# Performance work log

Measured on AMD Instinct MI355X. Metric: run time of the kernel, lower is better.

## Reference

```python
import jax, jax.numpy as jnp
import numpy as np

B, S, D, H, L, DFF, NA = 128, 52, 1024, 16, 8, 4096, 1000
DK = D // H
KTOP = int((1.0 - 0.9) * S)  # per-row top-k kept before threshold = 5
EPS = 1e-5
SCALE = 1.0 / np.sqrt(DK).astype(np.float32)


def setup_inputs() -> dict:
    key = jax.random.key(0)
    ks = jax.random.split(key, 30)
    # token grid: channels 0,1 in [0,50) so only designated positions match special tokens
    x = jax.random.randint(ks[0], (B, S, 3), 0, 50).astype(jnp.int32)
    act = jax.random.randint(ks[1], (B, S), 0, NA).astype(jnp.int32)
    x = x.at[..., 2].set(act)
    x = x.at[:, 0].set(jnp.array([100, 0, 1], jnp.int32))    # SOS
    x = x.at[:, 26].set(jnp.array([100, 0, 2], jnp.int32))   # SEP
    x = x.at[:, 48:].set(jnp.array([100, 0, 0], jnp.int32))  # PAD tail

    def n(k, shape, scale=0.02):
        return (jax.random.normal(k, shape) * scale).astype(jnp.float32)

    return dict(
        x=x,
        action_emb=n(ks[2], (NA, D), 1.0),
        sep_token=n(ks[3], (D,), 1.0),
        bn_gamma=jnp.ones((S,), jnp.float32),
        bn_beta=jnp.zeros((S,), jnp.float32),
        Wq=n(ks[4], (L, D, D)), bq=jnp.zeros((L, D), jnp.float32),
        Wk=n(ks[5], (L, D, D)), bk=jnp.zeros((L, D), jnp.float32),
        Wv=n(ks[6], (L, D, D)), bv=jnp.zeros((L, D), jnp.float32),
        Wo=n(ks[7], (L, D, D)), bo=jnp.zeros((L, D), jnp.float32),
        W1=n(ks[8], (L, DFF, D)), b1=jnp.zeros((L, DFF), jnp.float32),
        W2=n(ks[9], (L, D, DFF)), b2=jnp.zeros((L, D), jnp.float32),
        ln1_g=jnp.ones((L, D), jnp.float32), ln1_b=jnp.zeros((L, D), jnp.float32),
        ln2_g=jnp.ones((L, D), jnp.float32), ln2_b=jnp.zeros((L, D), jnp.float32),
        Wout=n(ks[10], (3, D)), bout=jnp.zeros((3,), jnp.float32),
    )


def _ln(x, g, b):
    m = x.mean(-1, keepdims=True)
    v = x.var(-1, keepdims=True)
    return (x - m) * jax.lax.rsqrt(v + EPS) * g + b


def reference(x, action_emb, sep_token, bn_gamma, bn_beta,
              Wq, bq, Wk, bk, Wv, bv, Wo, bo,
              W1, b1, W2, b2, ln1_g, ln1_b, ln2_g, ln2_b, Wout, bout):
    PAD = jnp.array([100, 0, 0], x.dtype)
    SEP = jnp.array([100, 0, 2], x.dtype)
    pad = jnp.all(x == PAD, -1)            # [B,S]
    sep = jnp.all(x == SEP, -1)            # [B,S]
    valid = ~pad                            # attend only to non-pad keys

    # token-scatter embedding: sep positions -> sep_token, everything else -> action embedding
    h = jnp.where(sep[..., None], sep_token, action_emb[x[..., 2]])  # [B,S,D]

    # BatchNorm1d(52) over seq-as-channel dim (training-mode batch stats)
    mu = h.mean((0, 2), keepdims=True)
    var = h.var((0, 2), keepdims=True)
    h = (h - mu) * jax.lax.rsqrt(var + EPS) * bn_gamma[None, :, None] + bn_beta[None, :, None]

    for l in range(L):
        q = (h @ Wq[l].T + bq[l]).reshape(B, S, H, DK).transpose(0, 2, 1, 3)
        k = (h @ Wk[l].T + bk[l]).reshape(B, S, H, DK).transpose(0, 2, 1, 3)
        v = (h @ Wv[l].T + bv[l]).reshape(B, S, H, DK).transpose(0, 2, 1, 3)
        scores = jnp.einsum('bhqd,bhkd->bhqk', q, k) * SCALE       # [B,H,S,S]
        scores = jnp.where(valid[:, None, None, :], scores, -1e9)
        thr = jax.lax.top_k(scores, KTOP)[0][..., -1:]              # per-row k-th largest
        sparse = scores * (scores >= thr).astype(scores.dtype)      # zero out sub-threshold
        attn = jax.nn.softmax(sparse, axis=-1)
        o = jnp.einsum('bhqk,bhkd->bhqd', attn, v).transpose(0, 2, 1, 3).reshape(B, S, D)
        o = o @ Wo[l].T + bo[l]
        h = _ln(h + o, ln1_g[l], ln1_b[l])
        f = jax.nn.relu(h @ W1[l].T + b1[l]) @ W2[l].T + b2[l]
        h = _ln(h + f, ln2_g[l], ln2_b[l])

    y = h @ Wout.T + bout                                           # [B,S,3]
    return y[:, -1]
```

## Files before the change

### kernel.cpp

```cpp
#include <hip/hip_runtime.h>
#include <cstddef>
#include <cstdint>

#define B_    128
#define S_    52
#define D_    1024
#define H_    16
#define L_    8
#define DFF_  4096
#define DK_   64
#define T_    (B_*S_)
#define EPS_  1e-5f
#define SCALE_ 0.125f

typedef unsigned short ushortx4 __attribute__((ext_vector_type(4)));
typedef short  bf16x8 __attribute__((ext_vector_type(8)));
typedef float  f32x4  __attribute__((ext_vector_type(4)));

__device__ __forceinline__ unsigned short f2b(float f) {
  unsigned int u = __builtin_bit_cast(unsigned int, f);
  u = u + 0x7fffu + ((u >> 16) & 1u);
  return (unsigned short)(u >> 16);
}
__device__ __forceinline__ float b2f(unsigned short b) {
  unsigned int u = ((unsigned int)b) << 16;
  return __builtin_bit_cast(float, u);
}
__device__ __forceinline__ void gload16(const void* g, void* l) {
  __builtin_amdgcn_global_load_lds((const __attribute__((address_space(1))) unsigned int*)g,
      (__attribute__((address_space(3))) unsigned int*)l, 16, 0, 0);
}

__global__ __launch_bounds__(256) void k_embed(const int* __restrict__ x,
    const float* __restrict__ aemb, const float* __restrict__ sept,
    float* __restrict__ h, float* __restrict__ part, int* __restrict__ mask)
{
  int row = blockIdx.x;
  int b = row / S_;
  int s = row - b * S_;
  const int* xr = x + (size_t)row * 3;
  int x0 = xr[0], x1 = xr[1], x2 = xr[2];
  bool issep = (x0 == 100) && (x1 == 0) && (x2 == 2);
  bool ispad = (x0 == 100) && (x1 == 0) && (x2 == 0);
  int t = threadIdx.x;
  if (t == 0) mask[row] = ispad ? 0 : 1;
  const float* src = issep ? sept : (aemb + (size_t)x2 * D_);
  size_t base = (size_t)row * D_;
  float s1 = 0.f, s2 = 0.f;
#pragma unroll
  for (int i = 0; i < 4; ++i) {
    int d = t + i * 256;
    float v = src[d];
    h[base + d] = v;
    s1 += v;
    s2 += v * v;
  }
#pragma unroll
  for (int off = 32; off; off >>= 1) {
    s1 += __shfl_down(s1, off);
    s2 += __shfl_down(s2, off);
  }
  __shared__ float red[8];
  int lane = t & 63, wid = t >> 6;
  if (lane == 0) { red[wid] = s1; red[4 + wid] = s2; }
  __syncthreads();
  if (t == 0) {
    part[(size_t)s * B_ + b]        = red[0] + red[1] + red[2] + red[3];
    part[(size_t)(S_ + s) * B_ + b] = red[4] + red[5] + red[6] + red[7];
  }
}

__global__ __launch_bounds__(128) void k_bn_reduce(const float* __restrict__ part,
                                                   float* __restrict__ stats)
{
  int s = blockIdx.x;
  int t = threadIdx.x;
  float s1 = part[(size_t)s * B_ + t];
  float s2 = part[(size_t)(S_ + s) * B_ + t];
#pragma unroll
  for (int off = 32; off; off >>= 1) {
    s1 += __shfl_down(s1, off);
    s2 += __shfl_down(s2, off);
  }
  __shared__ float red[4];
  int lane = t & 63, wid = t >> 6;
  if (lane == 0) { red[wid] = s1; red[2 + wid] = s2; }
  __syncthreads();
  if (t == 0) {
    stats[s]      = red[0] + red[1];
    stats[S_ + s] = red[2] + red[3];
  }
}

__global__ __launch_bounds__(256) void k_bn_apply(float* __restrict__ h,
    const float* __restrict__ stats, const float* __restrict__ g,
    const float* __restrict__ bb, unsigned short* __restrict__ hb)
{
  int row = blockIdx.x;
  int s = row % S_;
  const float cnt = (float)(B_ * D_);
  float mu  = stats[s] / cnt;
  float var = stats[S_ + s] / cnt - mu * mu;
  float sc  = rsqrtf(var + EPS_) * g[s];
  float off = bb[s] - mu * sc;
  size_t base = (size_t)row * D_;
  int t = threadIdx.x;
#pragma unroll
  for (int i = 0; i < 4; ++i) {
    int d = t + i * 256;
    float v = h[base + d] * sc + off;
    h[base + d] = v;
    hb[base + d] = f2b(v);
  }
}

__global__ __launch_bounds__(256) void k_wconv(
    const float* __restrict__ wq, const float* __restrict__ wk,
    const float* __restrict__ wv, const float* __restrict__ wo,
    const float* __restrict__ w1, const float* __restrict__ w2,
    unsigned short* __restrict__ out)
{
  const size_t DD = (size_t)D_ * D_;
  const size_t DF = (size_t)DFF_ * D_;
  const size_t total = 4 * DD + 2 * DF;
  size_t stride = (size_t)gridDim.x * 256 * 4;
  for (size_t i = ((size_t)blockIdx.x * 256 + threadIdx.x) * 4; i < total; i += stride) {
    const float* src; size_t off;
    if      (i < DD)          { src = wq; off = i; }
    else if (i < 2 * DD)      { src = wk; off = i - DD; }
    else if (i < 3 * DD)      { src = wv; off = i - 2 * DD; }
    else if (i < 4 * DD)      { src = wo; off = i - 3 * DD; }
    else if (i < 4 * DD + DF) { src = w1; off = i - 4 * DD; }
    else                      { src = w2; off = i - 4 * DD - DF; }
    float4 v = *reinterpret_cast<const float4*>(src + off);
    ushortx4 o = { f2b(v.x), f2b(v.y), f2b(v.z), f2b(v.w) };
    *reinterpret_cast<ushortx4*>(out + i) = o;
  }
}

__global__ __launch_bounds__(256) void k_bcat(const float* __restrict__ bq,
    const float* __restrict__ bk, const float* __restrict__ bv,
    float* __restrict__ out)
{
  int i = blockIdx.x * 256 + threadIdx.x;
  int l = i / 3072, j = i - l * 3072;
  float v = (j < D_) ? bq[l * D_ + j] : (j < 2 * D_) ? bk[l * D_ + j - D_]
                                                     : bv[l * D_ + j - 2 * D_];
  out[i] = v;
}

template<int RELU, int OUTBF16>
__global__ __launch_bounds__(256) void k_gemm_bf16(
    const unsigned short* __restrict__ A, const unsigned short* __restrict__ Wt,
    const float* __restrict__ bias, void* __restrict__ C,
    int M, int N, int K, int ldc)
{
  __shared__ unsigned short As[128][32];
  __shared__ unsigned short Bs[128][32];
  int t = threadIdx.x;
  int lane = t & 63;
  int wid = t >> 6;
  int bm = blockIdx.y * 128;
  int bn = blockIdx.x * 128;
  int wr = wid >> 1, wc = wid & 1;

  const unsigned short* Ag = A + (size_t)(bm + wid * 32 + (lane >> 2)) * K + (lane & 3) * 8;
  const unsigned short* Bg = Wt + (size_t)(bn + wid * 32 + (lane >> 2)) * K + (lane & 3) * 8;

  f32x4 acc[4][4] = {};
  int fr = lane & 15;
  int kc = lane >> 4;

  for (int kt = 0; kt < K; kt += 32) {
#pragma unroll
    for (int j = 0; j < 2; ++j) {
      gload16(Ag + (size_t)j * 16 * K + kt, &As[wid * 32 + j * 16][0]);
      gload16(Bg + (size_t)j * 16 * K + kt, &Bs[wid * 32 + j * 16][0]);
    }
    __syncthreads();
    bf16x8 af[4], bfv[4];
#pragma unroll
    for (int m = 0; m < 4; ++m)
      af[m] = *reinterpret_cast<const bf16x8*>(&As[wr * 64 + m * 16 + fr][kc * 8]);
#pragma unroll
    for (int n = 0; n < 4; ++n)
      bfv[n] = *reinterpret_cast<const bf16x8*>(&Bs[wc * 64 + n * 16 + fr][kc * 8]);
#pragma unroll
    for (int m = 0; m < 4; ++m)
#pragma unroll
      for (int n = 0; n < 4; ++n)
        acc[m][n] = __builtin_amdgcn_mfma_f32_16x16x32_bf16(af[m], bfv[n], acc[m][n], 0, 0, 0);
    __syncthreads();
  }

  int fq = lane >> 4;
#pragma unroll
  for (int n = 0; n < 4; ++n) {
    int col = bn + wc * 64 + n * 16 + fr;
    float bv = bias[col];
#pragma unroll
    for (int m = 0; m < 4; ++m) {
      int row = bm + wr * 64 + m * 16 + fq * 4;
#pragma unroll
      for (int j = 0; j < 4; ++j) {
        float v = acc[m][n][j] + bv;
        if (RELU) v = fmaxf(v, 0.f);
        if (OUTBF16)
          ((unsigned short*)C)[(size_t)(row + j) * ldc + col] = f2b(v);
        else
          ((float*)C)[(size_t)(row + j) * ldc + col] = v;
      }
    }
  }
}

__global__ __launch_bounds__(64) void k_attn(const unsigned short* __restrict__ qkv,
    const int* __restrict__ mask, unsigned short* __restrict__ ao)
{
  __shared__ float sc[64][68];
  __shared__ unsigned short ph[64][68];
  __shared__ unsigned short plo[64][68];
  __shared__ unsigned short vT[64][68];
  __shared__ float dnm[64];

  int blk = blockIdx.x;
  int b = blk >> 4, hh = blk & 15;
  int l = threadIdx.x;
  int cl = l & 15, kg = l >> 4;
  const unsigned short* base = qkv + (size_t)(b * S_) * 3072 + hh * 64;

  {
    const unsigned short* vp = base + 2048 + l;
#pragma unroll 4
    for (int k = 0; k < S_; ++k)
      vT[l][k] = vp[(size_t)k * 3072];
#pragma unroll
    for (int k = S_; k < 64; ++k) vT[l][k] = 0;
  }

  bf16x8 qa[4][2], kb[4][2];
#pragma unroll
  for (int mi = 0; mi < 4; ++mi) {
    int row = mi * 16 + cl;
    bool ok = (row < S_);
    const unsigned short* qp = base + (size_t)row * 3072 + kg * 8;
#pragma unroll
    for (int ks = 0; ks < 2; ++ks) {
      bf16x8 z = {};
      qa[mi][ks] = ok ? *reinterpret_cast<const bf16x8*>(qp + ks * 32) : z;
      kb[mi][ks] = ok ? *reinterpret_cast<const bf16x8*>(qp + 1024 + ks * 32) : z;
    }
  }

  f32x4 acc[4][4] = {};
#pragma unroll
  for (int ks = 0; ks < 2; ++ks)
#pragma unroll
    for (int mi = 0; mi < 4; ++mi)
#pragma unroll
      for (int ci = 0; ci < 4; ++ci)
        acc[mi][ci] = __builtin_amdgcn_mfma_f32_16x16x32_bf16(qa[mi][ks], kb[ci][ks], acc[mi][ci], 0, 0, 0);

  int vld[4];
#pragma unroll
  for (int ci = 0; ci < 4; ++ci) {
    int col = ci * 16 + cl;
    vld[ci] = (col < S_) ? mask[b * S_ + col] : 0;
  }
#pragma unroll
  for (int mi = 0; mi < 4; ++mi)
#pragma unroll
    for (int ci = 0; ci < 4; ++ci)
#pragma unroll
      for (int j = 0; j < 4; ++j)
        sc[mi * 16 + kg * 4 + j][ci * 16 + cl] = vld[ci] ? acc[mi][ci][j] * SCALE_ : -1e9f;

  __syncthreads();

  if (l < S_) {
    float v0 = -3e38f, v1 = -3e38f, v2 = -3e38f, v3 = -3e38f, v4 = -3e38f;
    const float4* rp = reinterpret_cast<const float4*>(&sc[l][0]);
#pragma unroll
    for (int c4 = 0; c4 < 13; ++c4) {
      float4 x = rp[c4];
      float xs[4] = { x.x, x.y, x.z, x.w };
#pragma unroll
      for (int u = 0; u < 4; ++u) {
        float xv = xs[u];
        if      (xv > v0) { v4 = v3; v3 = v2; v2 = v1; v1 = v0; v0 = xv; }
        else if (xv > v1) { v4 = v3; v3 = v2; v2 = v1; v1 = xv; }
        else if (xv > v2) { v4 = v3; v3 = v2; v2 = xv; }
        else if (xv > v3) { v4 = v3; v3 = xv; }
        else if (xv > v4) { v4 = xv; }
      }
    }
    float thr = v4;
    float m = fmaxf(v0, 0.f);
    float denom = 0.f;
    for (int c = 0; c < S_; ++c) {
      float xv = sc[l][c];
      float sp = (xv >= thr) ? xv : 0.f;
      float e = __expf(sp - m);
      denom += e;
      unsigned short hi = f2b(e);
      ph[l][c] = hi;
      plo[l][c] = f2b(e - b2f(hi));
    }
#pragma unroll
    for (int c = S_; c < 64; ++c) { ph[l][c] = 0; plo[l][c] = 0; }
    dnm[l] = 1.f / denom;
  }
  __syncthreads();

  f32x4 o[4][4] = {};
#pragma unroll
  for (int ks = 0; ks < 2; ++ks) {
    bf16x8 vf[4];
#pragma unroll
    for (int di = 0; di < 4; ++di)
      vf[di] = *reinterpret_cast<const bf16x8*>(&vT[di * 16 + cl][ks * 32 + kg * 8]);
#pragma unroll
    for (int mi = 0; mi < 4; ++mi) {
      bf16x8 ahi = *reinterpret_cast<const bf16x8*>(&ph[mi * 16 + cl][ks * 32 + kg * 8]);
      bf16x8 alo = *reinterpret_cast<const bf16x8*>(&plo[mi * 16 + cl][ks * 32 + kg * 8]);
#pragma unroll
      for (int di = 0; di < 4; ++di) {
        o[mi][di] = __builtin_amdgcn_mfma_f32_16x16x32_bf16(ahi, vf[di], o[mi][di], 0, 0, 0);
        o[mi][di] = __builtin_amdgcn_mfma_f32_16x16x32_bf16(alo, vf[di], o[mi][di], 0, 0, 0);
      }
    }
  }

#pragma unroll
  for (int mi = 0; mi < 4; ++mi) {
    int row = mi * 16 + kg * 4;
    if (row < S_) {
#pragma unroll
      for (int j = 0; j < 4; ++j) {
        int r = row + j;
        float inv = dnm[r];
        unsigned short* aop = ao + (size_t)(b * S_ + r) * D_ + hh * DK_;
#pragma unroll
        for (int di = 0; di < 4; ++di)
          aop[di * 16 + cl] = f2b(o[mi][di][j] * inv);
      }
    }
  }
}

__global__ __launch_bounds__(256) void k_add_ln(float* __restrict__ h,
    const float* __restrict__ r, const float* __restrict__ g,
    const float* __restrict__ bb, unsigned short* __restrict__ hb)
{
  int row = blockIdx.x;
  size_t base = (size_t)row * D_;
  int t = threadIdx.x;
  float xs[4];
  float s1 = 0.f, s2 = 0.f;
#pragma unroll
  for (int i = 0; i < 4; ++i) {
    int d = t + i * 256;
    float xv = h[base + d] + r[base + d];
    xs[i] = xv;
    s1 += xv;
    s2 += xv * xv;
  }
#pragma unroll
  for (int off = 32; off; off >>= 1) {
    s1 += __shfl_down(s1, off);
    s2 += __shfl_down(s2, off);
  }
  __shared__ float red[8];
  int lane = t & 63, wid = t >> 6;
  if (lane == 0) { red[wid] = s1; red[4 + wid] = s2; }
  __syncthreads();
  if (t == 0) {
    red[0] = red[0] + red[1] + red[2] + red[3];
    red[4] = red[4] + red[5] + red[6] + red[7];
  }
  __syncthreads();
  float mean = red[0] / (float)D_;
  float var  = red[4] / (float)D_ - mean * mean;
  float inv  = rsqrtf(var + EPS_);
#pragma unroll
  for (int i = 0; i < 4; ++i) {
    int d = t + i * 256;
    float v = (xs[i] - mean) * inv * g[d] + bb[d];
    h[base + d] = v;
    hb[base + d] = f2b(v);
  }
}

__global__ __launch_bounds__(256) void k_final(const float* __restrict__ h,
    const float* __restrict__ Wout, const float* __restrict__ bout,
    float* __restrict__ y)
{
  int b = blockIdx.x;
  const float* hr = h + (size_t)(b * S_ + (S_ - 1)) * D_;
  int t = threadIdx.x;
  float p0 = 0.f, p1 = 0.f, p2 = 0.f;
  for (int d = t; d < D_; d += 256) {
    float xv = hr[d];
    p0 += xv * Wout[d];
    p1 += xv * Wout[D_ + d];
    p2 += xv * Wout[2 * D_ + d];
  }
#pragma unroll
  for (int off = 32; off; off >>= 1) {
    p0 += __shfl_down(p0, off);
    p1 += __shfl_down(p1, off);
    p2 += __shfl_down(p2, off);
  }
  __shared__ float red[12];
  int lane = t & 63, wid = t >> 6;
  if (lane == 0) { red[wid] = p0; red[4 + wid] = p1; red[8 + wid] = p2; }
  __syncthreads();
  if (t == 0) {
    y[b * 3 + 0] = red[0] + red[1] + red[2]  + red[3]  + bout[0];
    y[b * 3 + 1] = red[4] + red[5] + red[6]  + red[7]  + bout[1];
    y[b * 3 + 2] = red[8] + red[9] + red[10] + red[11] + bout[2];
  }
}

extern "C" void kernel_launch(void* const* d_in, const int* in_sizes, int n_in,
                              void* d_out, int out_size, void* d_ws, size_t ws_size,
                              hipStream_t stream)
{
  const int*   x    = (const int*)d_in[0];
  const float* aemb = (const float*)d_in[1];
  const float* sept = (const float*)d_in[2];
  const float* bng  = (const float*)d_in[3];
  const float* bnb  = (const float*)d_in[4];
  const float* Wq = (const float*)d_in[5];  const float* bq = (const float*)d_in[6];
  const float* Wk = (const float*)d_in[7];  const float* bk = (const float*)d_in[8];
  const float* Wv = (const float*)d_in[9];  const float* bv = (const float*)d_in[10];
  const float* Wo = (const float*)d_in[11]; const float* bo = (const float*)d_in[12];
  const float* W1 = (const float*)d_in[13]; const float* b1 = (const float*)d_in[14];
  const float* W2 = (const float*)d_in[15]; const float* b2 = (const float*)d_in[16];
  const float* ln1g = (const float*)d_in[17]; const float* ln1b = (const float*)d_in[18];
  const float* ln2g = (const float*)d_in[19]; const float* ln2b = (const float*)d_in[20];
  const float* Wout = (const float*)d_in[21]; const float* bout = (const float*)d_in[22];
  float* out = (float*)d_out;

  float* ws = (float*)d_ws;
  const size_t TD = (size_t)T_ * D_;
  const size_t DD = (size_t)D_ * D_;
  const size_t DF = (size_t)DFF_ * D_;
  float* h   = ws;
  float* tmp = ws + TD;
  unsigned short* hb   = (unsigned short*)(ws + 2 * TD);
  unsigned short* qkvb = (unsigned short*)(ws + 2 * TD + TD / 2);
  unsigned short* aob  = (unsigned short*)(ws + 4 * TD);
  unsigned short* ffb  = (unsigned short*)(ws + 4 * TD + TD / 2);
  unsigned short* wbuf = (unsigned short*)(ws + 6 * TD + TD / 2);
  float* bqkv = ws + 6 * TD + TD / 2 + (4 * DD + 2 * DF) / 2;
  float* stats = bqkv + L_ * 3072;
  float* part  = stats + 2 * S_;
  int*   mask  = (int*)(part + 2 * S_ * B_);

  k_embed<<<T_, 256, 0, stream>>>(x, aemb, sept, h, part, mask);
  k_bn_reduce<<<S_, 128, 0, stream>>>(part, stats);
  k_bn_apply<<<T_, 256, 0, stream>>>(h, stats, bng, bnb, hb);
  k_bcat<<<(L_ * 3072) / 256, 256, 0, stream>>>(bq, bk, bv, bqkv);

  for (int l = 0; l < L_; ++l) {
    k_wconv<<<3072, 256, 0, stream>>>(Wq + l * DD, Wk + l * DD, Wv + l * DD,
                                      Wo + l * DD, W1 + l * DF, W2 + l * DF, wbuf);
    k_gemm_bf16<0, 1><<<dim3(24, 52), 256, 0, stream>>>(hb, wbuf, bqkv + l * 3072,
        qkvb, T_, 3072, D_, 3072);
    k_attn<<<B_ * H_, 64, 0, stream>>>(qkvb, mask, aob);
    k_gemm_bf16<0, 0><<<dim3(8, 52), 256, 0, stream>>>(aob, wbuf + 3 * DD, bo + l * D_,
        tmp, T_, D_, D_, D_);
    k_add_ln<<<T_, 256, 0, stream>>>(h, tmp, ln1g + l * D_, ln1b + l * D_, hb);
    k_gemm_bf16<1, 1><<<dim3(32, 52), 256, 0, stream>>>(hb, wbuf + 4 * DD, b1 + l * DFF_,
        ffb, T_, DFF_, D_, DFF_);
    k_gemm_bf16<0, 0><<<dim3(8, 52), 256, 0, stream>>>(ffb, wbuf + 4 * DD + DF, b2 + l * D_,
        tmp, T_, D_, DFF_, D_);
    k_add_ln<<<T_, 256, 0, stream>>>(h, tmp, ln2g + l * D_, ln2b + l * D_, hb);
  }
  k_final<<<B_, 256, 0, stream>>>(h, Wout, bout, out);
}
```

Before: 2.943 ms.

## Replace GEMM with 256x128 triple-buffered, swizzled-LDS, XCD-remapped bf16 MFMA kernel

Replaces the 128x128, single-buffered bf16 GEMM (two barriers per 32-wide K step) with a 512-thread kernel. It computes 256x128 tiles using a 64-wide K step and a three-stage LDS ring, so global loads for step t+2 overlap MFMA work on step t, with one barrier per step. LDS rows are XOR-swizzled to avoid bank conflicts, and block IDs are remapped across groups of 8 for better L2 locality. It trades higher LDS use (144 KB) and lower occupancy, plus fewer blocks for the N=1024 GEMMs (208), for better latency hiding.

```diff
diff --git a/kernel.cpp b/kernel.cpp
--- a/kernel.cpp
+++ b/kernel.cpp
@@ -150,65 +150,108 @@
 }
 
 template<int RELU, int OUTBF16>
-__global__ __launch_bounds__(256) void k_gemm_bf16(
+__global__ __launch_bounds__(512) void k_gemm8(
     const unsigned short* __restrict__ A, const unsigned short* __restrict__ Wt,
     const float* __restrict__ bias, void* __restrict__ C,
-    int M, int N, int K, int ldc)
-{
-  __shared__ unsigned short As[128][32];
-  __shared__ unsigned short Bs[128][32];
-  int t = threadIdx.x;
-  int lane = t & 63;
-  int wid = t >> 6;
-  int bm = blockIdx.y * 128;
-  int bn = blockIdx.x * 128;
-  int wr = wid >> 1, wc = wid & 1;
-
-  const unsigned short* Ag = A + (size_t)(bm + wid * 32 + (lane >> 2)) * K + (lane & 3) * 8;
-  const unsigned short* Bg = Wt + (size_t)(bn + wid * 32 + (lane >> 2)) * K + (lane & 3) * 8;
+    int Mtiles, int Ntiles, int K, int ldc)
+{
+  __shared__ unsigned short lds[3 * 24576];
+  const int tid = threadIdx.x;
+  const int w = tid >> 6, l = tid & 63;
+
+  const int nwg = Mtiles * Ntiles;
+  int id = blockIdx.x;
+  int swz = (id & 7) * (nwg >> 3) + (id >> 3);
+  int bym = swz % Mtiles, bxn = swz / Mtiles;
+  const int bm = bym * 256, bn = bxn * 128;
+
+  const int srow = l >> 3;
+  const unsigned inrow = ((l & 7) << 4) ^ ((l & 0x38) << 1);
+  const char* gA = (const char*)A + (size_t)(bm + w * 32 + srow) * ((size_t)K * 2) + inrow;
+  const char* gB = (const char*)Wt + (size_t)(bn + w * 16 + srow) * ((size_t)K * 2) + inrow;
+  const size_t rj = (size_t)8 * K * 2;
+  const int ldsA0 = w * 2048;
+  const int ldsB0 = 16384 + w * 1024;
+
+#define STAGE8(tt, bb) do {                                   \
+    size_t kb = (size_t)(tt) * 128;                           \
+    unsigned short* la = lds + (bb) * 24576 + ldsA0;          \
+    unsigned short* lb = lds + (bb) * 24576 + ldsB0;          \
+    gload16(gA + kb,          la);                            \
+    gload16(gA + kb + rj,     la + 512);                      \
+    gload16(gA + kb + 2 * rj, la + 1024);                     \
+    gload16(gA + kb + 3 * rj, la + 1536);                     \
+    gload16(gB + kb,          lb);                            \
+    gload16(gB + kb + rj,     lb + 512);                      \
+  } while (0)
+
+  const int fr = l & 15, kg = l >> 4;
+  const int wr = w >> 1, wcn = w & 1;
+  const unsigned sw = (fr & 7) << 4;
+  const unsigned colk0 = ((unsigned)(kg * 16)) ^ sw;
+  const unsigned colk1 = ((unsigned)(64 + kg * 16)) ^ sw;
+  const unsigned aRow0 = (unsigned)(wr * 64 + fr) * 128;
+  const unsigned bRow0 = 32768u + (unsigned)(wcn * 64 + fr) * 128;
 
   f32x4 acc[4][4] = {};
-  int fr = lane & 15;
-  int kc = lane >> 4;
-
-  for (int kt = 0; kt < K; kt += 32) {
-#pragma unroll
-    for (int j = 0; j < 2; ++j) {
-      gload16(Ag + (size_t)j * 16 * K + kt, &As[wid * 32 + j * 16][0]);
-      gload16(Bg + (size_t)j * 16 * K + kt, &Bs[wid * 32 + j * 16][0]);
-    }
-    __syncthreads();
-    bf16x8 af[4], bfv[4];
-#pragma unroll
-    for (int m = 0; m < 4; ++m)
-      af[m] = *reinterpret_cast<const bf16x8*>(&As[wr * 64 + m * 16 + fr][kc * 8]);
-#pragma unroll
-    for (int n = 0; n < 4; ++n)
-      bfv[n] = *reinterpret_cast<const bf16x8*>(&Bs[wc * 64 + n * 16 + fr][kc * 8]);
-#pragma unroll
-    for (int m = 0; m < 4; ++m)
-#pragma unroll
-      for (int n = 0; n < 4; ++n)
-        acc[m][n] = __builtin_amdgcn_mfma_f32_16x16x32_bf16(af[m], bfv[n], acc[m][n], 0, 0, 0);
-    __syncthreads();
-  }
-
-  int fq = lane >> 4;
+  const int NT = K >> 6;
+
+  STAGE8(0, 0);
+  STAGE8(1, 1);
+  asm volatile("s_waitcnt vmcnt(6)" ::: "memory");
+  __builtin_amdgcn_sched_barrier(0);
+  __builtin_amdgcn_s_barrier();
+  __builtin_amdgcn_sched_barrier(0);
+
+  int cur = 0;
+  for (int t = 0; t < NT; ++t) {
+    if (t + 2 < NT) {
+      int sb = cur + 2; if (sb >= 3) sb -= 3;
+      STAGE8(t + 2, sb);
+    }
+    const char* bp = (const char*)(lds + cur * 24576);
+    bf16x8 bfr[4][2];
+#pragma unroll
+    for (int n = 0; n < 4; ++n) {
+      bfr[n][0] = *(const bf16x8*)(bp + bRow0 + n * 2048 + colk0);
+      bfr[n][1] = *(const bf16x8*)(bp + bRow0 + n * 2048 + colk1);
+    }
+#pragma unroll
+    for (int m = 0; m < 4; ++m) {
+      bf16x8 a0 = *(const bf16x8*)(bp + aRow0 + m * 2048 + colk0);
+      bf16x8 a1 = *(const bf16x8*)(bp + aRow0 + m * 2048 + colk1);
+#pragma unroll
+      for (int n = 0; n < 4; ++n) {
+        acc[m][n] = __builtin_amdgcn_mfma_f32_16x16x32_bf16(a0, bfr[n][0], acc[m][n], 0, 0, 0);
+        acc[m][n] = __builtin_amdgcn_mfma_f32_16x16x32_bf16(a1, bfr[n][1], acc[m][n], 0, 0, 0);
+      }
+    }
+    if (t + 1 < NT) {
+      if (t + 2 < NT) { asm volatile("s_waitcnt vmcnt(6)" ::: "memory"); }
+      else            { asm volatile("s_waitcnt vmcnt(0)" ::: "memory"); }
+      __builtin_amdgcn_sched_barrier(0);
+      __builtin_amdgcn_s_barrier();
+      __builtin_amdgcn_sched_barrier(0);
+    }
+    cur = (cur == 2) ? 0 : cur + 1;
+  }
+#undef STAGE8
+
 #pragma unroll
   for (int n = 0; n < 4; ++n) {
-    int col = bn + wc * 64 + n * 16 + fr;
+    int col = bn + wcn * 64 + n * 16 + fr;
     float bv = bias[col];
 #pragma unroll
     for (int m = 0; m < 4; ++m) {
-      int row = bm + wr * 64 + m * 16 + fq * 4;
+      int row0 = bm + wr * 64 + m * 16 + kg * 4;
 #pragma unroll
       for (int j = 0; j < 4; ++j) {
         float v = acc[m][n][j] + bv;
         if (RELU) v = fmaxf(v, 0.f);
         if (OUTBF16)
-          ((unsigned short*)C)[(size_t)(row + j) * ldc + col] = f2b(v);
+          ((unsigned short*)C)[(size_t)(row0 + j) * ldc + col] = f2b(v);
         else
-          ((float*)C)[(size_t)(row + j) * ldc + col] = v;
+          ((float*)C)[(size_t)(row0 + j) * ldc + col] = v;
       }
     }
   }
@@ -466,16 +509,16 @@
   for (int l = 0; l < L_; ++l) {
     k_wconv<<<3072, 256, 0, stream>>>(Wq + l * DD, Wk + l * DD, Wv + l * DD,
                                       Wo + l * DD, W1 + l * DF, W2 + l * DF, wbuf);
-    k_gemm_bf16<0, 1><<<dim3(24, 52), 256, 0, stream>>>(hb, wbuf, bqkv + l * 3072,
-        qkvb, T_, 3072, D_, 3072);
+    k_gemm8<0, 1><<<26 * 24, 512, 0, stream>>>(hb, wbuf, bqkv + l * 3072,
+        qkvb, 26, 24, 1024, 3072);
     k_attn<<<B_ * H_, 64, 0, stream>>>(qkvb, mask, aob);
-    k_gemm_bf16<0, 0><<<dim3(8, 52), 256, 0, stream>>>(aob, wbuf + 3 * DD, bo + l * D_,
-        tmp, T_, D_, D_, D_);
+    k_gemm8<0, 0><<<26 * 8, 512, 0, stream>>>(aob, wbuf + 3 * DD, bo + l * D_,
+        tmp, 26, 8, 1024, 1024);
     k_add_ln<<<T_, 256, 0, stream>>>(h, tmp, ln1g + l * D_, ln1b + l * D_, hb);
-    k_gemm_bf16<1, 1><<<dim3(32, 52), 256, 0, stream>>>(hb, wbuf + 4 * DD, b1 + l * DFF_,
-        ffb, T_, DFF_, D_, DFF_);
-    k_gemm_bf16<0, 0><<<dim3(8, 52), 256, 0, stream>>>(ffb, wbuf + 4 * DD + DF, b2 + l * D_,
-        tmp, T_, D_, DFF_, D_);
+    k_gemm8<1, 1><<<26 * 32, 512, 0, stream>>>(hb, wbuf + 4 * DD, b1 + l * DFF_,
+        ffb, 26, 32, 1024, 4096);
+    k_gemm8<0, 0><<<26 * 8, 512, 0, stream>>>(ffb, wbuf + 4 * DD + DF, b2 + l * D_,
+        tmp, 26, 8, 4096, 1024);
     k_add_ln<<<T_, 256, 0, stream>>>(h, tmp, ln2g + l * D_, ln2b + l * D_, hb);
   }
   k_final<<<B_, 256, 0, stream>>>(h, Wout, bout, out);
```

Result: faster. 2.636 ms (-10.4%).
